# Performance work log

Hardware: AMD Instinct MI355X
Metric: run time of the kernel (lower is better)

## Reference

```python
import jax, jax.numpy as jnp
import numpy as np

BINS = np.array([1, 2, 3, 4, 8, 16, 32, 64], dtype=np.int32)


def setup_inputs() -> dict:
    N, G, F, H, K = 1024, 620, 20, 150, 128
    D_in = 3 * G + F  # 1880
    key = jax.random.key(0)
    ks = jax.random.split(key, 10)
    g = jax.random.normal(ks[0], (N, G), dtype=jnp.float32)
    si = jax.random.normal(ks[1], (N,), dtype=jnp.float32)
    i1 = jnp.sort(jax.random.randint(ks[2], (N,), 0, 8192)).astype(jnp.int32)
    i2 = jnp.sort(jax.random.randint(ks[3], (N,), 0, 8192)).astype(jnp.int32)
    dist_emb = jax.random.normal(ks[4], (9, F), dtype=jnp.float32) * 0.02
    W1 = jax.random.normal(ks[5], (D_in, H), dtype=jnp.float32) * (1.0 / np.sqrt(D_in))
    b1 = jnp.zeros((H,), jnp.float32)
    W2 = jax.random.normal(ks[6], (H, H), dtype=jnp.float32) * (1.0 / np.sqrt(H))
    b2 = jnp.zeros((H,), jnp.float32)
    W3 = jax.random.normal(ks[7], (H, 1), dtype=jnp.float32) * (1.0 / np.sqrt(H))
    b3 = jnp.zeros((1,), jnp.float32)
    return {"g": g, "si": si, "i1": i1, "i2": i2, "dist_emb": dist_emb,
            "W1": W1, "b1": b1, "W2": W2, "b2": b2, "W3": W3, "b3": b3, "K": K}


def reference(g, si, i1, i2, dist_emb, W1, b1, W2, b2, W3, b3, K):
    # Dropout is inference-disabled; epsilon dummy antecedent appended as last column.
    N, G = g.shape
    # span n's antecedents are spans [max(0, n-K), n); lay out as [N, K] window
    j_idx = jnp.arange(N)[:, None] - K + jnp.arange(K)[None, :]  # [N, K]
    valid = j_idx >= 0
    j = jnp.clip(j_idx, 0, N - 1)
    g_j = g[j]                      # [N, K, G] ragged gather (masked dense)
    g_i = g[:, None, :]             # [N, 1, G]
    # distance feature: bin(i.i2 - j.i1) with idx = #bins <= d
    d = i2[:, None] - i1[j]         # [N, K]
    bin_idx = jnp.searchsorted(jnp.asarray(BINS), d, side='right')
    de = dist_emb[bin_idx]          # [N, K, F]
    pairs = jnp.concatenate(
        [jnp.broadcast_to(g_i, (N, K, G)), g_j, g_i * g_j, de], axis=-1)  # [N, K, 3G+F]
    h = jax.nn.relu(jnp.einsum('nkd,dh->nkh', pairs, W1) + b1)
    h = jax.nn.relu(jnp.einsum('nkh,hm->nkm', h, W2) + b2)
    s = (jnp.einsum('nkh,ho->nko', h, W3) + b3)[..., 0]  # [N, K]
    sij = si[:, None] + si[j] + s
    sij = jnp.where(valid, sij, 0.0)
    eps = jnp.zeros((N, 1), sij.dtype)  # epsilon dummy score
    return jnp.concatenate([sij, eps], axis=-1)  # [N, K+1]
```

## Files before the change

kernel.cpp:

```cpp
#include <hip/hip_runtime.h>
#include <hip/hip_bf16.h>
#include <stdint.h>

typedef __attribute__((ext_vector_type(8))) short short8;
typedef __attribute__((ext_vector_type(4))) float float4_t;

#define N_PTS 1024
#define G_DIM 620
#define G_PAD 640
#define F_DIM 20
#define H_DIM 150
#define H_PAD 160
#define K_WIN 128
#define OUT_C (K_WIN + 1)
#define BK 32
#define NSTEP 20
#define PSTR 80

__device__ __forceinline__ float bf2f(short u) {
  union { unsigned int i; float f; } x;
  x.i = ((unsigned int)(unsigned short)u) << 16;
  return x.f;
}
__device__ __forceinline__ short f2bf(float f) {
  union { float f; unsigned int i; } x; x.f = f;
  unsigned int u = x.i;
  u += 0x7FFFu + ((u >> 16) & 1u);
  return (short)(u >> 16);
}
__device__ __forceinline__ short f2bf_hw(float f) {
  __hip_bfloat16 h = __float2bfloat16(f);
  union { __hip_bfloat16 h; short s; } u; u.h = h;
  return u.s;
}
__device__ __forceinline__ void gload_lds16(const void* g, void* l) {
  __builtin_amdgcn_global_load_lds(
      (const __attribute__((address_space(1))) unsigned int*)g,
      (__attribute__((address_space(3))) unsigned int*)l, 16, 0, 0);
}

__global__ void prep_pack(const float* __restrict__ g, const float* __restrict__ W1,
                          const float* __restrict__ W2, const float* __restrict__ dist_emb,
                          short* __restrict__ g_bf, short* __restrict__ W1cT,
                          short* __restrict__ W1abT, short* __restrict__ W2T,
                          short* __restrict__ deWT) {
  __shared__ float lds[32 * 165];
  __shared__ float dw[9 * H_PAD];
  const int bx = blockIdx.x, tid = threadIdx.x;
  if (bx < 256) {
    const int n0 = bx * 4;
    for (int c = tid; c < 320; c += 256) {
      int r = c / 80, cc = c - r * 80;
      int n = n0 + r, d0 = cc * 8;
      short8 o;
      if (d0 + 8 <= G_DIM) {
        const float* src = g + n * G_DIM + d0;
        #pragma unroll
        for (int e = 0; e < 8; ++e) o[e] = f2bf(src[e]);
      } else {
        #pragma unroll
        for (int e = 0; e < 8; ++e) {
          int d = d0 + e;
          o[e] = (d < G_DIM) ? f2bf(g[n * G_DIM + d]) : (short)0;
        }
      }
      *(short8*)(g_bf + n * G_PAD + d0) = o;
    }
  } else if (bx < 316) {
    const int tb = bx - 256;
    const int third = tb / 20, dt = tb - third * 20;
    const int d0 = dt * 32;
    for (int c = tid; c < 1280; c += 256) {
      int dr = c / 40, ch4 = c - dr * 40;
      int dd = d0 + dr;
      int w1r = third * G_DIM + dd;
      #pragma unroll
      for (int e = 0; e < 4; ++e) {
        int h = ch4 * 4 + e;
        lds[dr * 165 + h] = (dd < G_DIM && h < H_DIM) ? W1[w1r * H_DIM + h] : 0.f;
      }
    }
    __syncthreads();
    short* outp = (third == 2) ? W1cT : (W1abT + third * H_PAD * G_PAD);
    for (int c = tid; c < 640; c += 256) {
      int h = c >> 2, ch = c & 3;
      short8 o;
      #pragma unroll
      for (int e = 0; e < 8; ++e) o[e] = f2bf(lds[(ch * 8 + e) * 165 + h]);
      *(short8*)(outp + h * G_PAD + d0 + ch * 8) = o;
    }
  } else if (bx < 320) {
    const int base = (bx - 316) * 6400;
    for (int c = tid; c < 6400; c += 256) {
      int q = base + c;
      int m = q / H_PAD, k = q - m * H_PAD;
      W2T[q] = (m < H_DIM && k < H_DIM) ? f2bf(W2[k * H_DIM + m]) : (short)0;
    }
  } else {
    for (int c = tid; c < 9 * H_PAD; c += 256) {
      int b = c / H_PAD, h = c - b * H_PAD;
      float acc = 0.f;
      if (h < H_DIM)
        for (int f = 0; f < F_DIM; ++f)
          acc += dist_emb[b * F_DIM + f] * W1[(3 * G_DIM + f) * H_DIM + h];
      dw[c] = acc;
    }
    __syncthreads();
    if (tid < H_PAD) {
      #pragma unroll
      for (int ch = 0; ch < 4; ++ch) {
        short8 o;
        #pragma unroll
        for (int e = 0; e < 8; ++e) {
          int kk = ch * 8 + e;
          o[e] = (kk < 9) ? f2bf(dw[kk * H_PAD + tid]) : (short)0;
        }
        *(short8*)(deWT + tid * 32 + ch * 8) = o;
      }
    }
  }
}

__global__ __launch_bounds__(256) void prep_uv_mfma(
    const short* __restrict__ g_bf, const short* __restrict__ W1abT,
    const float* __restrict__ b1, short* __restrict__ U_bf, float* __restrict__ V) {
  __shared__ __align__(16) char sA[64 * 128];
  __shared__ __align__(16) char sB[160 * 128];
  const int m0 = blockIdx.x * 64;
  const int yb = blockIdx.y * H_PAD;
  const int tid = threadIdx.x, lane = tid & 63, wid = tid >> 6;
  const int wm = wid >> 1, wn = wid & 1;
  const int lo4 = lane & 15, hi2 = lane >> 4;
  const int l8 = lane >> 3, c8 = lane & 7;
  const int xe = (c8 ^ (l8 & 7)) * 8;

  const float4_t fz = {0.f, 0.f, 0.f, 0.f};
  float4_t acc[2][5];
  #pragma unroll
  for (int a = 0; a < 2; ++a)
    #pragma unroll
    for (int b = 0; b < 5; ++b) acc[a][b] = fz;

  for (int step = 0; step < 10; ++step) {
    const int d0 = step * 64;
    #pragma unroll
    for (int cc = 0; cc < 2; ++cc) {
      int row = wid * 8 + cc * 32 + l8;
      gload_lds16(g_bf + (m0 + row) * G_PAD + d0 + xe, sA + (wid * 8 + cc * 32) * 128);
    }
    #pragma unroll
    for (int cc = 0; cc < 5; ++cc) {
      int row = wid * 8 + cc * 32 + l8;
      gload_lds16(W1abT + (yb + row) * G_PAD + d0 + xe, sB + (wid * 8 + cc * 32) * 128);
    }
    __syncthreads();
    #pragma unroll
    for (int ks = 0; ks < 2; ++ks) {
      const int kb = ks * 64 + 16 * hi2;
      short8 af[2], bq[5];
      #pragma unroll
      for (int mt = 0; mt < 2; ++mt) {
        int row = wm * 32 + mt * 16 + lo4;
        af[mt] = *((const short8*)(sA + row * 128 + (kb ^ ((row & 7) << 4))));
      }
      #pragma unroll
      for (int nt = 0; nt < 5; ++nt) {
        int row = wn * 80 + nt * 16 + lo4;
        bq[nt] = *((const short8*)(sB + row * 128 + (kb ^ ((row & 7) << 4))));
      }
      #pragma unroll
      for (int mt = 0; mt < 2; ++mt)
        #pragma unroll
        for (int nt = 0; nt < 5; ++nt)
          acc[mt][nt] = __builtin_amdgcn_mfma_f32_16x16x32_bf16(af[mt], bq[nt], acc[mt][nt], 0, 0, 0);
    }
    __syncthreads();
  }

  const bool isU = (blockIdx.y == 0);
  #pragma unroll
  for (int mt = 0; mt < 2; ++mt)
    #pragma unroll
    for (int r = 0; r < 4; ++r) {
      int m = m0 + wm * 32 + mt * 16 + hi2 * 4 + r;
      #pragma unroll
      for (int nt = 0; nt < 5; ++nt) {
        int h = wn * 80 + nt * 16 + lo4;
        float v = acc[mt][nt][r];
        if (isU) {
          v = (h < H_DIM) ? v + b1[h] : 0.f;
          U_bf[m * H_PAD + h] = f2bf(v);
        } else {
          V[m * H_PAD + h] = (h < H_DIM) ? v : 0.f;
        }
      }
    }
}

__global__ __launch_bounds__(256, 3) void pair_main(
    const short* __restrict__ g_bf, const short* __restrict__ W1cT,
    const short* __restrict__ W2T, const short* __restrict__ U_bf,
    const float* __restrict__ V, const short* __restrict__ deWT,
    const float* __restrict__ si, const int* __restrict__ i1,
    const int* __restrict__ i2, const float* __restrict__ W3,
    const float* __restrict__ b2, const float* __restrict__ b3,
    float* __restrict__ out) {
  __shared__ __align__(16) char smem[49152];
  __shared__ __align__(16) short gi_s[G_PAD];
  __shared__ float sj_s[K_WIN];
  __shared__ int bin_s[K_WIN];
  __shared__ float s_buf[2][K_WIN];

  char* const P0 = smem;
  char* const P1 = smem + 10240;
  char* const B0 = smem + 20480;
  char* const B1 = smem + 33280;
  char* const Hb = smem;

  const int bid = blockIdx.x;
  const int i = ((bid & 7) << 7) | (bid >> 3);
  const int tid = threadIdx.x;
  const int lane = tid & 63;
  const int wid = tid >> 6;
  const int wm = wid >> 1, wn = wid & 1;
  const int lo4 = lane & 15, hi2 = lane >> 4;
  const int rA = tid >> 2;
  const int cA = tid & 3;

  if (tid < G_PAD / 8)
    ((short8*)gi_s)[tid] = ((const short8*)(g_bf + i * G_PAD))[tid];
  if (tid < K_WIN) {
    int jr = i - K_WIN + tid, jc = jr < 0 ? 0 : jr;
    int d = i2[i] - i1[jc];
    bin_s[tid] = (d >= 1) + (d >= 2) + (d >= 3) + (d >= 4) +
                 (d >= 8) + (d >= 16) + (d >= 32) + (d >= 64);
    sj_s[tid] = si[jc];
  }
  __syncthreads();

  int jr0 = i - K_WIN + rA;        int jc0 = jr0 < 0 ? 0 : jr0;
  int jr1 = i - K_WIN + rA + 64;   int jc1 = jr1 < 0 ? 0 : jr1;
  const short* gpA0 = g_bf + jc0 * G_PAD + cA * 8;
  const short* gpA1 = g_bf + jc1 * G_PAD + cA * 8;
  const short* wb0 = W1cT + rA * G_PAD + cA * 8;
  const short* wb1 = W1cT + (rA + 64) * G_PAD + cA * 8;
  const short* wb2 = W1cT + (rA + 128) * G_PAD + cA * 8;

  short8 ra0, ra1, rgv, rb0, rb1, rb2;
  auto issue_loads = [&](int s) {
    if (s < NSTEP) {
      const int d0 = s * BK;
      rgv = *(const short8*)(gi_s + d0 + cA * 8);
      ra0 = *(const short8*)(gpA0 + d0);
      ra1 = *(const short8*)(gpA1 + d0);
      rb0 = *(const short8*)(wb0 + d0);
      rb1 = *(const short8*)(wb1 + d0);
      if (tid < 128) rb2 = *(const short8*)(wb2 + d0);
    } else {
      int bv0 = bin_s[rA], bv1 = bin_s[rA + 64];
      #pragma unroll
      for (int e = 0; e < 8; ++e) {
        int kk = cA * 8 + e;
        ra0[e] = (kk == bv0 || kk == 9) ? (short)0x3F80 : (short)0;
        ra1[e] = (kk == bv1 || kk == 9) ? (short)0x3F80 : (short)0;
        rgv[e] = (short)0x3F80;
      }
      rb0 = *(const short8*)(deWT + rA * BK + cA * 8);
      rb1 = *(const short8*)(deWT + (rA + 64) * BK + cA * 8);
      if (tid < 128) rb2 = *(const short8*)(deWT + (rA + 128) * BK + cA * 8);
    }
  };
  auto write_stage = [&](char* P, char* B) {
    short8 p0, p1;
    #pragma unroll
    for (int e = 0; e < 8; ++e) {
      p0[e] = f2bf_hw(bf2f(ra0[e]) * bf2f(rgv[e]));
      p1[e] = f2bf_hw(bf2f(ra1[e]) * bf2f(rgv[e]));
    }
    *(short8*)(P + rA * PSTR + cA * 16) = p0;
    *(short8*)(P + (rA + 64) * PSTR + cA * 16) = p1;
    *(short8*)(B + rA * PSTR + cA * 16) = rb0;
    *(short8*)(B + (rA + 64) * PSTR + cA * 16) = rb1;
    if (tid < 128) *(short8*)(B + (rA + 128) * PSTR + cA * 16) = rb2;
  };

  const float4_t fz = {0.f, 0.f, 0.f, 0.f};
  float4_t acc[4][5];
  #pragma unroll
  for (int a = 0; a < 4; ++a)
    #pragma unroll
    for (int b = 0; b < 5; ++b) acc[a][b] = fz;

  issue_loads(0);
  write_stage(P0, B0);

  for (int s = 0; s <= NSTEP; ++s) {
    char* Pc = (s & 1) ? P1 : P0;
    char* Bc = (s & 1) ? B1 : B0;
    char* Pn = (s & 1) ? P0 : P1;
    char* Bn = (s & 1) ? B0 : B1;
    __syncthreads();
    if (s == NSTEP) {
      if (tid < H_PAD) *(short*)(Bc + tid * PSTR + 18) = U_bf[i * H_PAD + tid];
      __syncthreads();
    }
    if (s < NSTEP) issue_loads(s + 1);
    {
      short8 af[4], bq[5];
      #pragma unroll
      for (int mt = 0; mt < 4; ++mt) {
        int row = wm * 64 + mt * 16 + lo4;
        af[mt] = *((const short8*)(Pc + row * PSTR + hi2 * 16));
      }
      #pragma unroll
      for (int nt = 0; nt < 5; ++nt) {
        int row = wn * 80 + nt * 16 + lo4;
        bq[nt] = *((const short8*)(Bc + row * PSTR + hi2 * 16));
      }
      #pragma unroll
      for (int mt = 0; mt < 4; ++mt)
        #pragma unroll
        for (int nt = 0; nt < 5; ++nt)
          acc[mt][nt] = __builtin_amdgcn_mfma_f32_16x16x32_bf16(af[mt], bq[nt], acc[mt][nt], 0, 0, 0);
    }
    if (s < NSTEP) write_stage(Pn, Bn);
  }
  __syncthreads();

  #pragma unroll
  for (int mt = 0; mt < 4; ++mt) {
    #pragma unroll
    for (int r = 0; r < 4; ++r) {
      int m = wm * 64 + mt * 16 + hi2 * 4 + r;
      int jr = i - K_WIN + m, jc = jr < 0 ? 0 : jr;
      const float* Vj = V + jc * H_PAD;
      #pragma unroll
      for (int nt = 0; nt < 5; ++nt) {
        int h = wn * 80 + nt * 16 + lo4;
        float val = acc[mt][nt][r] + Vj[h];
        val = (h < H_DIM) ? fmaxf(val, 0.f) : 0.f;
        int tile = h >> 6, hc = h & 63;
        int byte = tile * 16384 + m * 128 + ((hc * 2) ^ ((m & 7) << 4));
        *((short*)(Hb + byte)) = f2bf_hw(val);
      }
    }
  }
  {
    short8 z = {0, 0, 0, 0, 0, 0, 0, 0};
    for (int c = tid; c < 512; c += 256) {
      int row = c >> 2, cb = c & 3;
      int byte = 2 * 16384 + row * 128 + ((64 + cb * 16) ^ ((row & 7) << 4));
      *((short8*)(Hb + byte)) = z;
    }
  }
  __syncthreads();

  float4_t acc2[4][5];
  #pragma unroll
  for (int a = 0; a < 4; ++a)
    #pragma unroll
    for (int b = 0; b < 5; ++b) acc2[a][b] = fz;

  short8 bql[2][5];
  #pragma unroll
  for (int nt = 0; nt < 5; ++nt) {
    int row = wn * 80 + nt * 16 + lo4;
    bql[0][nt] = *(const short8*)(W2T + row * H_PAD + hi2 * 8);
  }
  #pragma unroll
  for (int ks = 0; ks < 5; ++ks) {
    const int cur = ks & 1;
    if (ks < 4) {
      #pragma unroll
      for (int nt = 0; nt < 5; ++nt) {
        int row = wn * 80 + nt * 16 + lo4;
        bql[cur ^ 1][nt] = *(const short8*)(W2T + row * H_PAD + (ks + 1) * BK + hi2 * 8);
      }
    }
    short8 af[4];
    #pragma unroll
    for (int mt = 0; mt < 4; ++mt) {
      int row = wm * 64 + mt * 16 + lo4;
      int kb = (ks & 1) * 64 + hi2 * 16;
      af[mt] = *((const short8*)(Hb + (ks >> 1) * 16384 + row * 128 + (kb ^ ((row & 7) << 4))));
    }
    #pragma unroll
    for (int mt = 0; mt < 4; ++mt)
      #pragma unroll
      for (int nt = 0; nt < 5; ++nt)
        acc2[mt][nt] = __builtin_amdgcn_mfma_f32_16x16x32_bf16(af[mt], bql[cur][nt], acc2[mt][nt], 0, 0, 0);
  }

  float sp[4][4];
  #pragma unroll
  for (int mt = 0; mt < 4; ++mt)
    #pragma unroll
    for (int r = 0; r < 4; ++r) sp[mt][r] = 0.f;

  #pragma unroll
  for (int nt = 0; nt < 5; ++nt) {
    int h = wn * 80 + nt * 16 + lo4;
    float w3 = (h < H_DIM) ? W3[h] : 0.f;
    float bb = (h < H_DIM) ? b2[h] : 0.f;
    #pragma unroll
    for (int mt = 0; mt < 4; ++mt)
      #pragma unroll
      for (int r = 0; r < 4; ++r) {
        float hv = fmaxf(acc2[mt][nt][r] + bb, 0.f);
        sp[mt][r] += hv * w3;
      }
  }
  #pragma unroll
  for (int mt = 0; mt < 4; ++mt)
    #pragma unroll
    for (int r = 0; r < 4; ++r) {
      float v = sp[mt][r];
      v += __shfl_xor(v, 1);
      v += __shfl_xor(v, 2);
      v += __shfl_xor(v, 4);
      v += __shfl_xor(v, 8);
      sp[mt][r] = v;
    }
  if (lo4 == 0) {
    #pragma unroll
    for (int mt = 0; mt < 4; ++mt)
      #pragma unroll
      for (int r = 0; r < 4; ++r) {
        int m = wm * 64 + mt * 16 + hi2 * 4 + r;
        s_buf[wn][m] = sp[mt][r];
      }
  }
  __syncthreads();

  if (tid < K_WIN) {
    int m = tid;
    int jr = i - K_WIN + m;
    float sij = si[i] + sj_s[m] + s_buf[0][m] + s_buf[1][m] + b3[0];
    out[i * OUT_C + m] = (jr >= 0) ? sij : 0.f;
  }
  if (tid == K_WIN) out[i * OUT_C + K_WIN] = 0.f;
}

extern "C" void kernel_launch(void* const* d_in, const int* in_sizes, int n_in,
                              void* d_out, int out_size, void* d_ws, size_t ws_size,
                              hipStream_t stream) {
  const float* g  = (const float*)d_in[0];
  const float* si = (const float*)d_in[1];
  const int*   i1 = (const int*)d_in[2];
  const int*   i2 = (const int*)d_in[3];
  const float* de = (const float*)d_in[4];
  const float* W1 = (const float*)d_in[5];
  const float* b1 = (const float*)d_in[6];
  const float* W2 = (const float*)d_in[7];
  const float* b2 = (const float*)d_in[8];
  const float* W3 = (const float*)d_in[9];
  const float* b3 = (const float*)d_in[10];
  float* out = (float*)d_out;

  char* ws = (char*)d_ws;
  short* g_bf  = (short*)(ws);
  short* W1cT  = (short*)(ws + 1310720);
  short* W1abT = (short*)(ws + 1515520);
  short* W2T   = (short*)(ws + 1925120);
  float* V     = (float*)(ws + 1976320);
  short* U_bf  = (short*)(ws + 2631680);
  short* deWT  = (short*)(ws + 2959360);

  prep_pack<<<321, 256, 0, stream>>>(g, W1, W2, de, g_bf, W1cT, W1abT, W2T, deWT);
  prep_uv_mfma<<<dim3(16, 2), 256, 0, stream>>>(g_bf, W1abT, b1, U_bf, V);
  pair_main<<<N_PTS, 256, 0, stream>>>(g_bf, W1cT, W2T, U_bf, V, deWT,
                                       si, i1, i2, W3, b2, b3, out);
}
```

Measured before the change: 80.53 us.

## Merge prep kernels and stream W1c tiles via direct-to-LDS loads

The two prep kernels become one launch: the U/V projection blocks now read fp32 g and W1 directly and convert them in LDS, instead of waiting for a separate packing pass. In the main pair kernel, W1c tiles are staged with global_load_lds into swizzled 64-wide LDS buffers, double-buffered. The g_i*g_j product is now computed in registers from fp32 g_i, with no separate LDS staging of the products. The distance-embedding and U bias step becomes a separate final MFMA stage with one-hot operands built in registers. This removes a launch and LDS traffic, but the fused prep blocks redo the g conversion and W1 transposes per block.

Measured after the change: 223.2 us. +177.1%, slower.

```diff
diff --git a/kernel.cpp b/kernel.cpp
--- a/kernel.cpp
+++ b/kernel.cpp
@@ -13,9 +13,6 @@
 #define H_PAD 160
 #define K_WIN 128
 #define OUT_C (K_WIN + 1)
-#define BK 32
-#define NSTEP 20
-#define PSTR 80
 
 __device__ __forceinline__ float bf2f(short u) {
   union { unsigned int i; float f; } x;
@@ -39,14 +36,15 @@
       (__attribute__((address_space(3))) unsigned int*)l, 16, 0, 0);
 }
 
-__global__ void prep_pack(const float* __restrict__ g, const float* __restrict__ W1,
-                          const float* __restrict__ W2, const float* __restrict__ dist_emb,
-                          short* __restrict__ g_bf, short* __restrict__ W1cT,
-                          short* __restrict__ W1abT, short* __restrict__ W2T,
-                          short* __restrict__ deWT) {
-  __shared__ float lds[32 * 165];
-  __shared__ float dw[9 * H_PAD];
+__global__ void prep_all(const float* __restrict__ g, const float* __restrict__ W1,
+                         const float* __restrict__ W2, const float* __restrict__ dist_emb,
+                         const float* __restrict__ b1,
+                         short* __restrict__ g_bf, short* __restrict__ W1cT,
+                         short* __restrict__ W2T, short* __restrict__ deWT_g,
+                         short* __restrict__ U_bf, float* __restrict__ V) {
+  __shared__ __align__(16) char psm[32256];
   const int bx = blockIdx.x, tid = threadIdx.x;
+
   if (bx < 256) {
     const int n0 = bx * 4;
     for (int c = tid; c < 320; c += 256) {
@@ -66,37 +64,36 @@
       }
       *(short8*)(g_bf + n * G_PAD + d0) = o;
     }
-  } else if (bx < 316) {
-    const int tb = bx - 256;
-    const int third = tb / 20, dt = tb - third * 20;
+  } else if (bx < 276) {
+    float* lds = (float*)psm;
+    const int dt = bx - 256;
     const int d0 = dt * 32;
     for (int c = tid; c < 1280; c += 256) {
       int dr = c / 40, ch4 = c - dr * 40;
       int dd = d0 + dr;
-      int w1r = third * G_DIM + dd;
       #pragma unroll
       for (int e = 0; e < 4; ++e) {
         int h = ch4 * 4 + e;
-        lds[dr * 165 + h] = (dd < G_DIM && h < H_DIM) ? W1[w1r * H_DIM + h] : 0.f;
+        lds[dr * 165 + h] = (dd < G_DIM && h < H_DIM) ? W1[(2 * G_DIM + dd) * H_DIM + h] : 0.f;
       }
     }
     __syncthreads();
-    short* outp = (third == 2) ? W1cT : (W1abT + third * H_PAD * G_PAD);
     for (int c = tid; c < 640; c += 256) {
       int h = c >> 2, ch = c & 3;
       short8 o;
       #pragma unroll
       for (int e = 0; e < 8; ++e) o[e] = f2bf(lds[(ch * 8 + e) * 165 + h]);
-      *(short8*)(outp + h * G_PAD + d0 + ch * 8) = o;
-    }
-  } else if (bx < 320) {
-    const int base = (bx - 316) * 6400;
+      *(short8*)(W1cT + h * G_PAD + d0 + ch * 8) = o;
+    }
+  } else if (bx < 280) {
+    const int base = (bx - 276) * 6400;
     for (int c = tid; c < 6400; c += 256) {
       int q = base + c;
       int m = q / H_PAD, k = q - m * H_PAD;
       W2T[q] = (m < H_DIM && k < H_DIM) ? f2bf(W2[k * H_DIM + m]) : (short)0;
     }
-  } else {
+  } else if (bx == 280) {
+    float* dw = (float*)psm;
     for (int c = tid; c < 9 * H_PAD; c += 256) {
       int b = c / H_PAD, h = c - b * H_PAD;
       float acc = 0.f;
@@ -106,115 +103,115 @@
       dw[c] = acc;
     }
     __syncthreads();
-    if (tid < H_PAD) {
-      #pragma unroll
-      for (int ch = 0; ch < 4; ++ch) {
-        short8 o;
+    for (int c = tid; c < H_PAD * 8; c += 256) {
+      int row = c >> 3, ch = c & 7;
+      short8 o;
+      #pragma unroll
+      for (int e = 0; e < 8; ++e) {
+        int kk = ch * 8 + e;
+        o[e] = (kk < 9) ? f2bf(dw[kk * H_PAD + row]) : (short)0;
+      }
+      *(short8*)(deWT_g + row * 64 + ch * 8) = o;
+    }
+  } else {
+    char* AsB = psm;
+    char* WtT = psm + 64 * 144;
+    const int uvb = bx - 281;
+    const int y = uvb >> 4;
+    const int m0 = (uvb & 15) * 64;
+    const int lane = tid & 63, wid = tid >> 6;
+    const int wm = wid >> 1, wn = wid & 1;
+    const int lo4 = lane & 15, hi2 = lane >> 4;
+    const float* W1y = W1 + y * G_DIM * H_DIM;
+
+    const float4_t fz = {0.f, 0.f, 0.f, 0.f};
+    float4_t acc[2][5];
+    #pragma unroll
+    for (int a = 0; a < 2; ++a)
+      #pragma unroll
+      for (int b = 0; b < 5; ++b) acc[a][b] = fz;
+
+    for (int step = 0; step < 10; ++step) {
+      const int d0 = step * 64;
+      __syncthreads();
+      {
+        int r = tid >> 2, q = tid & 3;
+        const float* gr = g + (m0 + r) * G_DIM;
+        short8 o0, o1;
         #pragma unroll
         for (int e = 0; e < 8; ++e) {
-          int kk = ch * 8 + e;
-          o[e] = (kk < 9) ? f2bf(dw[kk * H_PAD + tid]) : (short)0;
-        }
-        *(short8*)(deWT + tid * 32 + ch * 8) = o;
-      }
-    }
-  }
-}
-
-__global__ __launch_bounds__(256) void prep_uv_mfma(
-    const short* __restrict__ g_bf, const short* __restrict__ W1abT,
-    const float* __restrict__ b1, short* __restrict__ U_bf, float* __restrict__ V) {
-  __shared__ __align__(16) char sA[64 * 128];
-  __shared__ __align__(16) char sB[160 * 128];
-  const int m0 = blockIdx.x * 64;
-  const int yb = blockIdx.y * H_PAD;
-  const int tid = threadIdx.x, lane = tid & 63, wid = tid >> 6;
-  const int wm = wid >> 1, wn = wid & 1;
-  const int lo4 = lane & 15, hi2 = lane >> 4;
-  const int l8 = lane >> 3, c8 = lane & 7;
-  const int xe = (c8 ^ (l8 & 7)) * 8;
-
-  const float4_t fz = {0.f, 0.f, 0.f, 0.f};
-  float4_t acc[2][5];
-  #pragma unroll
-  for (int a = 0; a < 2; ++a)
-    #pragma unroll
-    for (int b = 0; b < 5; ++b) acc[a][b] = fz;
-
-  for (int step = 0; step < 10; ++step) {
-    const int d0 = step * 64;
-    #pragma unroll
-    for (int cc = 0; cc < 2; ++cc) {
-      int row = wid * 8 + cc * 32 + l8;
-      gload_lds16(g_bf + (m0 + row) * G_PAD + d0 + xe, sA + (wid * 8 + cc * 32) * 128);
-    }
-    #pragma unroll
-    for (int cc = 0; cc < 5; ++cc) {
-      int row = wid * 8 + cc * 32 + l8;
-      gload_lds16(W1abT + (yb + row) * G_PAD + d0 + xe, sB + (wid * 8 + cc * 32) * 128);
-    }
-    __syncthreads();
-    #pragma unroll
-    for (int ks = 0; ks < 2; ++ks) {
-      const int kb = ks * 64 + 16 * hi2;
-      short8 af[2], bq[5];
-      #pragma unroll
-      for (int mt = 0; mt < 2; ++mt) {
-        int row = wm * 32 + mt * 16 + lo4;
-        af[mt] = *((const short8*)(sA + row * 128 + (kb ^ ((row & 7) << 4))));
-      }
-      #pragma unroll
-      for (int nt = 0; nt < 5; ++nt) {
-        int row = wn * 80 + nt * 16 + lo4;
-        bq[nt] = *((const short8*)(sB + row * 128 + (kb ^ ((row & 7) << 4))));
-      }
-      #pragma unroll
-      for (int mt = 0; mt < 2; ++mt)
-        #pragma unroll
-        for (int nt = 0; nt < 5; ++nt)
-          acc[mt][nt] = __builtin_amdgcn_mfma_f32_16x16x32_bf16(af[mt], bq[nt], acc[mt][nt], 0, 0, 0);
-    }
-    __syncthreads();
-  }
-
-  const bool isU = (blockIdx.y == 0);
-  #pragma unroll
-  for (int mt = 0; mt < 2; ++mt)
-    #pragma unroll
-    for (int r = 0; r < 4; ++r) {
-      int m = m0 + wm * 32 + mt * 16 + hi2 * 4 + r;
-      #pragma unroll
-      for (int nt = 0; nt < 5; ++nt) {
-        int h = wn * 80 + nt * 16 + lo4;
-        float v = acc[mt][nt][r];
-        if (isU) {
-          v = (h < H_DIM) ? v + b1[h] : 0.f;
-          U_bf[m * H_PAD + h] = f2bf(v);
-        } else {
-          V[m * H_PAD + h] = (h < H_DIM) ? v : 0.f;
-        }
-      }
-    }
+          int d = d0 + q * 16 + e;
+          o0[e] = (d < G_DIM) ? f2bf(gr[d]) : (short)0;
+          int d2 = d + 8;
+          o1[e] = (d2 < G_DIM) ? f2bf(gr[d2]) : (short)0;
+        }
+        *(short8*)(AsB + r * 144 + q * 32) = o0;
+        *(short8*)(AsB + r * 144 + q * 32 + 16) = o1;
+      }
+      for (int c = tid; c < 64 * 160; c += 256) {
+        int dr = c / 160, h = c - dr * 160;
+        int d = d0 + dr;
+        float w = (h < H_DIM && d < G_DIM) ? W1y[d * H_DIM + h] : 0.f;
+        *(short*)(WtT + h * 144 + dr * 2) = f2bf(w);
+      }
+      __syncthreads();
+      #pragma unroll
+      for (int ks = 0; ks < 2; ++ks) {
+        const int kb = ks * 64 + hi2 * 16;
+        short8 af[2], bq[5];
+        #pragma unroll
+        for (int mt = 0; mt < 2; ++mt) {
+          int row = wm * 32 + mt * 16 + lo4;
+          af[mt] = *((const short8*)(AsB + row * 144 + kb));
+        }
+        #pragma unroll
+        for (int nt = 0; nt < 5; ++nt) {
+          int row = wn * 80 + nt * 16 + lo4;
+          bq[nt] = *((const short8*)(WtT + row * 144 + kb));
+        }
+        #pragma unroll
+        for (int mt = 0; mt < 2; ++mt)
+          #pragma unroll
+          for (int nt = 0; nt < 5; ++nt)
+            acc[mt][nt] = __builtin_amdgcn_mfma_f32_16x16x32_bf16(af[mt], bq[nt], acc[mt][nt], 0, 0, 0);
+      }
+    }
+    #pragma unroll
+    for (int mt = 0; mt < 2; ++mt)
+      #pragma unroll
+      for (int r = 0; r < 4; ++r) {
+        int m = m0 + wm * 32 + mt * 16 + hi2 * 4 + r;
+        #pragma unroll
+        for (int nt = 0; nt < 5; ++nt) {
+          int h = wn * 80 + nt * 16 + lo4;
+          float v = acc[mt][nt][r];
+          if (y == 0) {
+            v = (h < H_DIM) ? v + b1[h] : 0.f;
+            U_bf[m * H_PAD + h] = f2bf(v);
+          } else {
+            V[m * H_PAD + h] = (h < H_DIM) ? v : 0.f;
+          }
+        }
+      }
+  }
 }
 
 __global__ __launch_bounds__(256, 3) void pair_main(
-    const short* __restrict__ g_bf, const short* __restrict__ W1cT,
-    const short* __restrict__ W2T, const short* __restrict__ U_bf,
-    const float* __restrict__ V, const short* __restrict__ deWT,
-    const float* __restrict__ si, const int* __restrict__ i1,
-    const int* __restrict__ i2, const float* __restrict__ W3,
-    const float* __restrict__ b2, const float* __restrict__ b3,
-    float* __restrict__ out) {
+    const float* __restrict__ g, const short* __restrict__ g_bf,
+    const short* __restrict__ W1cT, const short* __restrict__ W2T,
+    const short* __restrict__ U_bf, const float* __restrict__ V,
+    const short* __restrict__ deWT_g, const float* __restrict__ si,
+    const int* __restrict__ i1, const int* __restrict__ i2,
+    const float* __restrict__ W3, const float* __restrict__ b2,
+    const float* __restrict__ b3, float* __restrict__ out) {
   __shared__ __align__(16) char smem[49152];
-  __shared__ __align__(16) short gi_s[G_PAD];
+  __shared__ __align__(16) float gi_sf[G_PAD];
   __shared__ float sj_s[K_WIN];
-  __shared__ int bin_s[K_WIN];
+  __shared__ unsigned char bin_su[K_WIN];
   __shared__ float s_buf[2][K_WIN];
 
-  char* const P0 = smem;
-  char* const P1 = smem + 10240;
-  char* const B0 = smem + 20480;
-  char* const B1 = smem + 33280;
+  char* const B0 = smem;
+  char* const B1 = smem + 20480;
   char* const Hb = smem;
 
   const int bid = blockIdx.x;
@@ -224,64 +221,41 @@
   const int wid = tid >> 6;
   const int wm = wid >> 1, wn = wid & 1;
   const int lo4 = lane & 15, hi2 = lane >> 4;
-  const int rA = tid >> 2;
-  const int cA = tid & 3;
-
-  if (tid < G_PAD / 8)
-    ((short8*)gi_s)[tid] = ((const short8*)(g_bf + i * G_PAD))[tid];
+  const int l8 = lane >> 3, c8 = lane & 7;
+  const int xe = (c8 ^ (l8 & 7)) * 8;
+
+  if (tid < 160) {
+    int c = tid;
+    float4_t v;
+    if (c < 155) v = *(const float4_t*)(g + i * G_DIM + c * 4);
+    else { v.x = v.y = v.z = v.w = 0.f; }
+    *(float4_t*)(gi_sf + c * 4) = v;
+  }
   if (tid < K_WIN) {
     int jr = i - K_WIN + tid, jc = jr < 0 ? 0 : jr;
     int d = i2[i] - i1[jc];
-    bin_s[tid] = (d >= 1) + (d >= 2) + (d >= 3) + (d >= 4) +
-                 (d >= 8) + (d >= 16) + (d >= 32) + (d >= 64);
+    bin_su[tid] = (unsigned char)((d >= 1) + (d >= 2) + (d >= 3) + (d >= 4) +
+                                  (d >= 8) + (d >= 16) + (d >= 32) + (d >= 64));
     sj_s[tid] = si[jc];
   }
   __syncthreads();
 
-  int jr0 = i - K_WIN + rA;        int jc0 = jr0 < 0 ? 0 : jr0;
-  int jr1 = i - K_WIN + rA + 64;   int jc1 = jr1 < 0 ? 0 : jr1;
-  const short* gpA0 = g_bf + jc0 * G_PAD + cA * 8;
-  const short* gpA1 = g_bf + jc1 * G_PAD + cA * 8;
-  const short* wb0 = W1cT + rA * G_PAD + cA * 8;
-  const short* wb1 = W1cT + (rA + 64) * G_PAD + cA * 8;
-  const short* wb2 = W1cT + (rA + 128) * G_PAD + cA * 8;
-
-  short8 ra0, ra1, rgv, rb0, rb1, rb2;
-  auto issue_loads = [&](int s) {
-    if (s < NSTEP) {
-      const int d0 = s * BK;
-      rgv = *(const short8*)(gi_s + d0 + cA * 8);
-      ra0 = *(const short8*)(gpA0 + d0);
-      ra1 = *(const short8*)(gpA1 + d0);
-      rb0 = *(const short8*)(wb0 + d0);
-      rb1 = *(const short8*)(wb1 + d0);
-      if (tid < 128) rb2 = *(const short8*)(wb2 + d0);
-    } else {
-      int bv0 = bin_s[rA], bv1 = bin_s[rA + 64];
-      #pragma unroll
-      for (int e = 0; e < 8; ++e) {
-        int kk = cA * 8 + e;
-        ra0[e] = (kk == bv0 || kk == 9) ? (short)0x3F80 : (short)0;
-        ra1[e] = (kk == bv1 || kk == 9) ? (short)0x3F80 : (short)0;
-        rgv[e] = (short)0x3F80;
-      }
-      rb0 = *(const short8*)(deWT + rA * BK + cA * 8);
-      rb1 = *(const short8*)(deWT + (rA + 64) * BK + cA * 8);
-      if (tid < 128) rb2 = *(const short8*)(deWT + (rA + 128) * BK + cA * 8);
-    }
-  };
-  auto write_stage = [&](char* P, char* B) {
-    short8 p0, p1;
-    #pragma unroll
-    for (int e = 0; e < 8; ++e) {
-      p0[e] = f2bf_hw(bf2f(ra0[e]) * bf2f(rgv[e]));
-      p1[e] = f2bf_hw(bf2f(ra1[e]) * bf2f(rgv[e]));
-    }
-    *(short8*)(P + rA * PSTR + cA * 16) = p0;
-    *(short8*)(P + (rA + 64) * PSTR + cA * 16) = p1;
-    *(short8*)(B + rA * PSTR + cA * 16) = rb0;
-    *(short8*)(B + (rA + 64) * PSTR + cA * 16) = rb1;
-    if (tid < 128) *(short8*)(B + (rA + 128) * PSTR + cA * 16) = rb2;
+  const short* gA[4];
+  int bv[4];
+  #pragma unroll
+  for (int mt = 0; mt < 4; ++mt) {
+    int row = wm * 64 + mt * 16 + lo4;
+    int jr = i - K_WIN + row, jc = jr < 0 ? 0 : jr;
+    gA[mt] = g_bf + jc * G_PAD + hi2 * 8;
+    bv[mt] = bin_su[row];
+  }
+
+  auto stageB = [&](const short* src, int sstride, char* B) {
+    #pragma unroll
+    for (int cc = 0; cc < 5; ++cc) {
+      int row = wid * 8 + cc * 32 + l8;
+      gload_lds16(src + row * sstride + xe, B + (wid * 8 + cc * 32) * 128);
+    }
   };
 
   const float4_t fz = {0.f, 0.f, 0.f, 0.f};
@@ -291,31 +265,40 @@
     #pragma unroll
     for (int b = 0; b < 5; ++b) acc[a][b] = fz;
 
-  issue_loads(0);
-  write_stage(P0, B0);
-
-  for (int s = 0; s <= NSTEP; ++s) {
-    char* Pc = (s & 1) ? P1 : P0;
+  stageB(W1cT, G_PAD, B0);
+
+  for (int s = 0; s < 10; ++s) {
     char* Bc = (s & 1) ? B1 : B0;
-    char* Pn = (s & 1) ? P0 : P1;
     char* Bn = (s & 1) ? B0 : B1;
     __syncthreads();
-    if (s == NSTEP) {
-      if (tid < H_PAD) *(short*)(Bc + tid * PSTR + 18) = U_bf[i * H_PAD + tid];
-      __syncthreads();
-    }
-    if (s < NSTEP) issue_loads(s + 1);
-    {
-      short8 af[4], bq[5];
+    short8 gj[4][2];
+    #pragma unroll
+    for (int mt = 0; mt < 4; ++mt)
+      #pragma unroll
+      for (int ks = 0; ks < 2; ++ks)
+        gj[mt][ks] = *(const short8*)(gA[mt] + s * 64 + ks * 32);
+    if (s < 9) stageB(W1cT + (s + 1) * 64, G_PAD, Bn);
+    else       stageB(deWT_g, 64, Bn);
+    #pragma unroll
+    for (int ks = 0; ks < 2; ++ks) {
+      const float* gis = gi_sf + s * 64 + ks * 32 + hi2 * 8;
+      float4_t g0 = *(const float4_t*)(gis);
+      float4_t g1 = *(const float4_t*)(gis + 4);
+      short8 af[4];
       #pragma unroll
       for (int mt = 0; mt < 4; ++mt) {
-        int row = wm * 64 + mt * 16 + lo4;
-        af[mt] = *((const short8*)(Pc + row * PSTR + hi2 * 16));
-      }
+        #pragma unroll
+        for (int e = 0; e < 4; ++e) {
+          af[mt][e]     = f2bf_hw(bf2f(gj[mt][ks][e])     * g0[e]);
+          af[mt][e + 4] = f2bf_hw(bf2f(gj[mt][ks][e + 4]) * g1[e]);
+        }
+      }
+      const int kb = ks * 64 + hi2 * 16;
+      short8 bq[5];
       #pragma unroll
       for (int nt = 0; nt < 5; ++nt) {
         int row = wn * 80 + nt * 16 + lo4;
-        bq[nt] = *((const short8*)(Bc + row * PSTR + hi2 * 16));
+        bq[nt] = *((const short8*)(Bc + row * 128 + (kb ^ ((row & 7) << 4))));
       }
       #pragma unroll
       for (int mt = 0; mt < 4; ++mt)
@@ -323,7 +306,40 @@
         for (int nt = 0; nt < 5; ++nt)
           acc[mt][nt] = __builtin_amdgcn_mfma_f32_16x16x32_bf16(af[mt], bq[nt], acc[mt][nt], 0, 0, 0);
     }
-    if (s < NSTEP) write_stage(Pn, Bn);
+  }
+
+  {
+    char* Bc = B0;
+    __syncthreads();
+    if (tid < H_PAD) {
+      int row = tid;
+      *(short*)(Bc + row * 128 + (18 ^ ((row & 7) << 4))) = U_bf[i * H_PAD + row];
+    }
+    __syncthreads();
+    #pragma unroll
+    for (int ks = 0; ks < 2; ++ks) {
+      short8 af[4];
+      #pragma unroll
+      for (int mt = 0; mt < 4; ++mt) {
+        #pragma unroll
+        for (int e = 0; e < 8; ++e) {
+          int k = ks * 32 + hi2 * 8 + e;
+          af[mt][e] = (k == bv[mt] || k == 9) ? (short)0x3F80 : (short)0;
+        }
+      }
+      const int kb = ks * 64 + hi2 * 16;
+      short8 bq[5];
+      #pragma unroll
+      for (int nt = 0; nt < 5; ++nt) {
+        int row = wn * 80 + nt * 16 + lo4;
+        bq[nt] = *((const short8*)(Bc + row * 128 + (kb ^ ((row & 7) << 4))));
+      }
+      #pragma unroll
+      for (int mt = 0; mt < 4; ++mt)
+        #pragma unroll
+        for (int nt = 0; nt < 5; ++nt)
+          acc[mt][nt] = __builtin_amdgcn_mfma_f32_16x16x32_bf16(af[mt], bq[nt], acc[mt][nt], 0, 0, 0);
+    }
   }
   __syncthreads();
 
@@ -374,7 +390,7 @@
       #pragma unroll
       for (int nt = 0; nt < 5; ++nt) {
         int row = wn * 80 + nt * 16 + lo4;
-        bql[cur ^ 1][nt] = *(const short8*)(W2T + row * H_PAD + (ks + 1) * BK + hi2 * 8);
+        bql[cur ^ 1][nt] = *(const short8*)(W2T + row * H_PAD + (ks + 1) * 32 + hi2 * 8);
       }
     }
     short8 af[4];
@@ -458,16 +474,14 @@
   float* out = (float*)d_out;
 
   char* ws = (char*)d_ws;
-  short* g_bf  = (short*)(ws);
-  short* W1cT  = (short*)(ws + 1310720);
-  short* W1abT = (short*)(ws + 1515520);
-  short* W2T   = (short*)(ws + 1925120);
-  float* V     = (float*)(ws + 1976320);
-  short* U_bf  = (short*)(ws + 2631680);
-  short* deWT  = (short*)(ws + 2959360);
-
-  prep_pack<<<321, 256, 0, stream>>>(g, W1, W2, de, g_bf, W1cT, W1abT, W2T, deWT);
-  prep_uv_mfma<<<dim3(16, 2), 256, 0, stream>>>(g_bf, W1abT, b1, U_bf, V);
-  pair_main<<<N_PTS, 256, 0, stream>>>(g_bf, W1cT, W2T, U_bf, V, deWT,
+  short* g_bf   = (short*)(ws);
+  short* W1cT   = (short*)(ws + 1310720);
+  short* W2T    = (short*)(ws + 1515520);
+  short* deWT_g = (short*)(ws + 1566720);
+  float* V      = (float*)(ws + 1587200);
+  short* U_bf   = (short*)(ws + 2242560);
+
+  prep_all<<<313, 256, 0, stream>>>(g, W1, W2, de, b1, g_bf, W1cT, W2T, deWT_g, U_bf, V);
+  pair_main<<<N_PTS, 256, 0, stream>>>(g, g_bf, W1cT, W2T, U_bf, V, deWT_g,
                                        si, i1, i2, W3, b2, b3, out);
 }
```
